# Performance work log

Measured on AMD Instinct MI355X. Metric: run time of the kernel, lower is better.

Reference implementation:

```python
import jax, jax.numpy as jnp
import numpy as np

NEG_INF = -1e30


def setup_inputs() -> dict:
    key = jax.random.key(0)
    k1, k2, k3 = jax.random.split(key, 3)
    B, L, D = 32, 4096, 1024
    sequence = jax.random.normal(k1, (B, L, D), dtype=jnp.float32)
    vector = jax.random.normal(k2, (B, D), dtype=jnp.float32)
    sequence_mask = jax.random.randint(k3, (B, L), 0, 2, dtype=jnp.int32)
    return {"sequence": sequence, "vector": vector, "sequence_mask": sequence_mask}


def reference(sequence, vector, sequence_mask):
    # DotProduct similarity: score[b,l] = <sequence[b,l,:], vector[b,:]>
    scores = jnp.einsum("bld,bd->bl", sequence, vector)
    mask = sequence_mask.astype(scores.dtype)
    # masked softmax over the sequence length dimension
    masked_scores = jnp.where(mask > 0, scores, NEG_INF)
    weights = jax.nn.softmax(masked_scores, axis=-1)
    # attention pooling: weighted sum of sequence positions -> [B, D]
    pooled = jnp.einsum("bl,bld->bd", weights, sequence)
    return pooled, weights
```

## Files before the change

### kernel.cpp

```cpp
#include <hip/hip_runtime.h>
#include <math.h>

constexpr int B = 32;
constexpr int L = 4096;
constexpr int D = 1024;
constexpr float NEG_INF = -1e30f;

constexpr int CH  = 128;
constexpr int RPW = L / CH;

using f32x4 = __attribute__((ext_vector_type(4))) float;

constexpr size_t WS_SCORES = 0;
constexpr size_t WS_PM     = WS_SCORES + (size_t)B * L;
constexpr size_t WS_PL     = WS_PM + (size_t)B * CH;
constexpr size_t WS_PAD    = WS_PL + (size_t)B * CH;
constexpr size_t WS_PACC   = WS_PAD + 2 * B;

__global__ __launch_bounds__(256, 4) void pass1_kernel(
    const float* __restrict__ seq, const float* __restrict__ vec,
    const int* __restrict__ mask, float* __restrict__ scores,
    float* __restrict__ pm, float* __restrict__ pl, float* __restrict__ pacc)
{
    const int wave = blockIdx.x * 4 + (threadIdx.x >> 6);
    const int lane = threadIdx.x & 63;
    const int b = wave >> 7;
    const int c = wave & (CH - 1);
    const int l0 = c * RPW;

    const f32x4* v4 = (const f32x4*)(vec + (size_t)b * D);
    const f32x4 v0 = v4[lane], v1 = v4[lane + 64], v2 = v4[lane + 128], v3 = v4[lane + 192];

    float m = -INFINITY, lsum = 0.f;
    f32x4 a0 = {0,0,0,0}, a1 = {0,0,0,0}, a2 = {0,0,0,0}, a3 = {0,0,0,0};

    const f32x4* srow = (const f32x4*)(seq + ((size_t)b * L + l0) * D);
    const int rowbase = b * L + l0;

    for (int it = 0; it < RPW / 2; ++it) {
        const int2 mk = *(const int2*)(mask + rowbase + it * 2);

        const f32x4* p0 = srow + (size_t)(it * 2) * (D / 4);
        const f32x4* p1 = p0 + (D / 4);
        f32x4 s00 = __builtin_nontemporal_load(p0 + lane);
        f32x4 s01 = __builtin_nontemporal_load(p0 + lane + 64);
        f32x4 s02 = __builtin_nontemporal_load(p0 + lane + 128);
        f32x4 s03 = __builtin_nontemporal_load(p0 + lane + 192);
        f32x4 s10 = __builtin_nontemporal_load(p1 + lane);
        f32x4 s11 = __builtin_nontemporal_load(p1 + lane + 64);
        f32x4 s12 = __builtin_nontemporal_load(p1 + lane + 128);
        f32x4 s13 = __builtin_nontemporal_load(p1 + lane + 192);

        f32x4 d0v = s00 * v0 + s01 * v1 + s02 * v2 + s03 * v3;
        f32x4 d1v = s10 * v0 + s11 * v1 + s12 * v2 + s13 * v3;
        float dot0 = d0v.x + d0v.y + d0v.z + d0v.w;
        float dot1 = d1v.x + d1v.y + d1v.z + d1v.w;

        #pragma unroll
        for (int off = 32; off; off >>= 1) {
            dot0 += __shfl_xor(dot0, off, 64);
            dot1 += __shfl_xor(dot1, off, 64);
        }

        const float sc0 = (mk.x > 0) ? dot0 : NEG_INF;
        const float sc1 = (mk.y > 0) ? dot1 : NEG_INF;

        const float mNew = fmaxf(fmaxf(sc0, sc1), m);
        if (mNew > m) {
            const float scale = __expf(m - mNew);
            lsum *= scale;
            a0 *= scale; a1 *= scale; a2 *= scale; a3 *= scale;
            m = mNew;
        }
        const float p0w = __expf(sc0 - m);
        const float p1w = __expf(sc1 - m);
        lsum += p0w + p1w;
        a0 += p0w * s00; a1 += p0w * s01; a2 += p0w * s02; a3 += p0w * s03;
        a0 += p1w * s10; a1 += p1w * s11; a2 += p1w * s12; a3 += p1w * s13;

        if (lane == 0) *(float2*)(scores + rowbase + it * 2) = make_float2(sc0, sc1);
    }

    f32x4* aout = (f32x4*)(pacc + (size_t)wave * D);
    aout[lane] = a0; aout[lane + 64] = a1; aout[lane + 128] = a2; aout[lane + 192] = a3;
    if (lane == 0) { pm[wave] = m; pl[wave] = lsum; }
}

__global__ __launch_bounds__(128) void combine_kernel(
    const float* __restrict__ pm, const float* __restrict__ pl,
    const float* __restrict__ pacc, const float* __restrict__ scores,
    float* __restrict__ pooled, float* __restrict__ out_w)
{
    const int b  = blockIdx.x;
    const int y  = blockIdx.y;
    const int ds = y * 128;
    const int t  = threadIdx.x;

    __shared__ float red[128];
    __shared__ float wgt[128];

    const float mc = pm[b * CH + t];
    const float lc = pl[b * CH + t];

    red[t] = mc; __syncthreads();
    #pragma unroll
    for (int s = 64; s; s >>= 1) { if (t < s) red[t] = fmaxf(red[t], red[t + s]); __syncthreads(); }
    const float M = red[0];
    __syncthreads();

    const float e = __expf(mc - M);
    wgt[t] = e;
    red[t] = lc * e; __syncthreads();
    #pragma unroll
    for (int s = 64; s; s >>= 1) { if (t < s) red[t] += red[t + s]; __syncthreads(); }
    const float denom = red[0];
    const float inv = 1.f / denom;

    float acc = 0.f;
    const float* base = pacc + (size_t)b * CH * D + ds + t;
    #pragma unroll 16
    for (int c = 0; c < CH; ++c)
        acc += base[(size_t)c * D] * wgt[c];
    pooled[b * D + ds + t] = acc * inv;

    const int l0 = y * 512;
    const f32x4 s4 = ((const f32x4*)(scores + (size_t)b * L + l0))[t];
    f32x4 w;
    w.x = __expf(s4.x - M) * inv;
    w.y = __expf(s4.y - M) * inv;
    w.z = __expf(s4.z - M) * inv;
    w.w = __expf(s4.w - M) * inv;
    ((f32x4*)(out_w + (size_t)b * L + l0))[t] = w;
}

extern "C" void kernel_launch(void* const* d_in, const int* in_sizes, int n_in,
                              void* d_out, int out_size, void* d_ws, size_t ws_size,
                              hipStream_t stream) {
    const float* seq  = (const float*)d_in[0];
    const float* vec  = (const float*)d_in[1];
    const int*   mask = (const int*)d_in[2];
    float* out = (float*)d_out;

    float* ws     = (float*)d_ws;
    float* scores = ws + WS_SCORES;
    float* pm     = ws + WS_PM;
    float* pl     = ws + WS_PL;
    float* pacc   = ws + WS_PACC;

    pass1_kernel<<<(B * CH) / 4, 256, 0, stream>>>(seq, vec, mask, scores, pm, pl, pacc);
    combine_kernel<<<dim3(B, D / 128), 128, 0, stream>>>(pm, pl, pacc, scores, out, out + B * D);
}
```

Before: 664.7 us.

## Skip loading masked sequence rows using a ballot bitmask of valid positions

Each wave builds a ballot bitmask of its 32 mask values and iterates only over unmasked rows, processing them two at a time with a single-row tail. Masked rows get zero softmax weight, so their 4 KB loads and dot products are dropped, cutting the HBM traffic of the dominant pass roughly in proportion to the masked fraction. Scores are collected per lane and written with one coalesced store instead of per-iteration lane-0 stores. The cost is data-dependent loop trip counts across waves. There is an edge case: a batch row that is fully masked now yields -inf maxima and no longer the uniform weights the reference gives.

```diff
diff --git a/kernel.cpp b/kernel.cpp
--- a/kernel.cpp
+++ b/kernel.cpp
@@ -31,55 +31,80 @@
     const f32x4* v4 = (const f32x4*)(vec + (size_t)b * D);
     const f32x4 v0 = v4[lane], v1 = v4[lane + 64], v2 = v4[lane + 128], v3 = v4[lane + 192];
 
+    const int rowbase = b * L + l0;
+    const f32x4* srow = (const f32x4*)(seq + (size_t)rowbase * D);
+
+    const int mv = mask[rowbase + (lane & 31)];
+    unsigned long long bits = __ballot((lane < 32) && (mv > 0));
+
     float m = -INFINITY, lsum = 0.f;
     f32x4 a0 = {0,0,0,0}, a1 = {0,0,0,0}, a2 = {0,0,0,0}, a3 = {0,0,0,0};
+    float myscore = NEG_INF;
 
-    const f32x4* srow = (const f32x4*)(seq + ((size_t)b * L + l0) * D);
-    const int rowbase = b * L + l0;
-
-    for (int it = 0; it < RPW / 2; ++it) {
-        const int2 mk = *(const int2*)(mask + rowbase + it * 2);
-
-        const f32x4* p0 = srow + (size_t)(it * 2) * (D / 4);
-        const f32x4* p1 = p0 + (D / 4);
+    while (bits) {
+        const int r0 = __builtin_ctzll(bits); bits &= bits - 1;
+        const f32x4* p0 = srow + (size_t)r0 * (D / 4);
         f32x4 s00 = __builtin_nontemporal_load(p0 + lane);
         f32x4 s01 = __builtin_nontemporal_load(p0 + lane + 64);
         f32x4 s02 = __builtin_nontemporal_load(p0 + lane + 128);
         f32x4 s03 = __builtin_nontemporal_load(p0 + lane + 192);
-        f32x4 s10 = __builtin_nontemporal_load(p1 + lane);
-        f32x4 s11 = __builtin_nontemporal_load(p1 + lane + 64);
-        f32x4 s12 = __builtin_nontemporal_load(p1 + lane + 128);
-        f32x4 s13 = __builtin_nontemporal_load(p1 + lane + 192);
 
-        f32x4 d0v = s00 * v0 + s01 * v1 + s02 * v2 + s03 * v3;
-        f32x4 d1v = s10 * v0 + s11 * v1 + s12 * v2 + s13 * v3;
-        float dot0 = d0v.x + d0v.y + d0v.z + d0v.w;
-        float dot1 = d1v.x + d1v.y + d1v.z + d1v.w;
+        if (bits) {
+            const int r1 = __builtin_ctzll(bits); bits &= bits - 1;
+            const f32x4* p1 = srow + (size_t)r1 * (D / 4);
+            f32x4 s10 = __builtin_nontemporal_load(p1 + lane);
+            f32x4 s11 = __builtin_nontemporal_load(p1 + lane + 64);
+            f32x4 s12 = __builtin_nontemporal_load(p1 + lane + 128);
+            f32x4 s13 = __builtin_nontemporal_load(p1 + lane + 192);
 
-        #pragma unroll
-        for (int off = 32; off; off >>= 1) {
-            dot0 += __shfl_xor(dot0, off, 64);
-            dot1 += __shfl_xor(dot1, off, 64);
+            f32x4 d0v = s00 * v0 + s01 * v1 + s02 * v2 + s03 * v3;
+            f32x4 d1v = s10 * v0 + s11 * v1 + s12 * v2 + s13 * v3;
+            float dot0 = d0v.x + d0v.y + d0v.z + d0v.w;
+            float dot1 = d1v.x + d1v.y + d1v.z + d1v.w;
+
+            #pragma unroll
+            for (int off = 32; off; off >>= 1) {
+                dot0 += __shfl_xor(dot0, off, 64);
+                dot1 += __shfl_xor(dot1, off, 64);
+            }
+
+            const float mNew = fmaxf(fmaxf(dot0, dot1), m);
+            if (mNew > m) {
+                const float scale = __expf(m - mNew);
+                lsum *= scale;
+                a0 *= scale; a1 *= scale; a2 *= scale; a3 *= scale;
+                m = mNew;
+            }
+            const float p0w = __expf(dot0 - m);
+            const float p1w = __expf(dot1 - m);
+            lsum += p0w + p1w;
+            a0 += p0w * s00; a1 += p0w * s01; a2 += p0w * s02; a3 += p0w * s03;
+            a0 += p1w * s10; a1 += p1w * s11; a2 += p1w * s12; a3 += p1w * s13;
+
+            if (lane == r0) myscore = dot0;
+            if (lane == r1) myscore = dot1;
+        } else {
+            f32x4 d0v = s00 * v0 + s01 * v1 + s02 * v2 + s03 * v3;
+            float dot0 = d0v.x + d0v.y + d0v.z + d0v.w;
+            #pragma unroll
+            for (int off = 32; off; off >>= 1)
+                dot0 += __shfl_xor(dot0, off, 64);
+
+            if (dot0 > m) {
+                const float scale = __expf(m - dot0);
+                lsum *= scale;
+                a0 *= scale; a1 *= scale; a2 *= scale; a3 *= scale;
+                m = dot0;
+            }
+            const float p = __expf(dot0 - m);
+            lsum += p;
+            a0 += p * s00; a1 += p * s01; a2 += p * s02; a3 += p * s03;
+
+            if (lane == r0) myscore = dot0;
         }
+    }
 
-        const float sc0 = (mk.x > 0) ? dot0 : NEG_INF;
-        const float sc1 = (mk.y > 0) ? dot1 : NEG_INF;
-
-        const float mNew = fmaxf(fmaxf(sc0, sc1), m);
-        if (mNew > m) {
-            const float scale = __expf(m - mNew);
-            lsum *= scale;
-            a0 *= scale; a1 *= scale; a2 *= scale; a3 *= scale;
-            m = mNew;
-        }
-        const float p0w = __expf(sc0 - m);
-        const float p1w = __expf(sc1 - m);
-        lsum += p0w + p1w;
-        a0 += p0w * s00; a1 += p0w * s01; a2 += p0w * s02; a3 += p0w * s03;
-        a0 += p1w * s10; a1 += p1w * s11; a2 += p1w * s12; a3 += p1w * s13;
-
-        if (lane == 0) *(float2*)(scores + rowbase + it * 2) = make_float2(sc0, sc1);
-    }
+    if (lane < 32) scores[rowbase + lane] = myscore;
 
     f32x4* aout = (f32x4*)(pacc + (size_t)wave * D);
     aout[lane] = a0; aout[lane + 64] = a1; aout[lane + 128] = a2; aout[lane + 192] = a3;
```

New measurement: 620.6 us. -6.6%, faster.
